# Kernel optimization log

Hardware: AMD Instinct MI355X
Metric: run time of the kernel (lower is better)

The kernel has to match this reference:

```python
import jax, jax.numpy as jnp
import numpy as np

N = 10000      # nodes
E = 160000     # edges
D_IN = 512
D_H = 512
P_DROP = 0.2


def _glorot(key, shape):
    lim = float(np.sqrt(6.0 / (shape[0] + shape[1])))
    return jax.random.uniform(key, shape, jnp.float32, -lim, lim)


def setup_inputs() -> dict:
    key = jax.random.key(0)
    ks = jax.random.split(key, 8)
    h = jax.random.normal(ks[0], (N, D_IN), jnp.float32)
    src = jax.random.randint(ks[1], (E,), 0, N)
    dst = jax.random.randint(ks[2], (E,), 0, N)
    edge_weight = jax.random.uniform(ks[3], (E,), jnp.float32)
    W0 = _glorot(ks[4], (D_IN, D_H))
    W1 = _glorot(ks[5], (D_H, D_H))
    W2 = _glorot(ks[6], (D_H, D_H))
    b0 = jnp.zeros((D_H,), jnp.float32)
    b1 = jnp.zeros((D_H,), jnp.float32)
    b2 = jnp.zeros((D_H,), jnp.float32)
    return dict(h=h, src=src, dst=dst, edge_weight=edge_weight,
                W0=W0, b0=b0, W1=W1, b1=b1, W2=W2, b2=b2)


def _dropout(x, key):
    keep = jax.random.bernoulli(key, 1.0 - P_DROP, x.shape)
    return jnp.where(keep, x / (1.0 - P_DROP), 0.0)


def _graph_conv(x, src, dst, ew, W, b, act):
    # DGL GraphConv, norm='both', weight=True, bias=True, with edge_weight.
    ones = jnp.ones((src.shape[0],), x.dtype)
    deg_out = jnp.maximum(jax.ops.segment_sum(ones, src, num_segments=N), 1.0)
    deg_in = jnp.maximum(jax.ops.segment_sum(ones, dst, num_segments=N), 1.0)
    x = x * (deg_out ** -0.5)[:, None]          # src norm
    msg = x[src] * ew[:, None]                  # [E, D] gather + edge weight
    agg = jax.ops.segment_sum(msg, dst, num_segments=N)  # scatter-add
    out = (agg @ W) * (deg_in ** -0.5)[:, None] + b
    return act(out) if act is not None else out


def reference(h, src, dst, edge_weight, W0, b0, W1, b1, W2, b2):
    dk = jax.random.split(jax.random.key(42), 3)
    x = _dropout(h, dk[0])
    x = _graph_conv(x, src, dst, edge_weight, W0, b0, jax.nn.elu)
    x = _dropout(x, dk[1])
    x = _graph_conv(x, src, dst, edge_weight, W1, b1, jax.nn.elu)
    x = _dropout(x, dk[2])
    x = _graph_conv(x, src, dst, edge_weight, W2, b2, None)
    return x
```

## Files before the change

### kernel.cpp

```cpp
#include <hip/hip_runtime.h>
#include <stdint.h>

#define N_NODES 10000
#define N_EDGES 160000
#define D 512
#define TOT (N_NODES * D)
#define NMASK (TOT / 32)
#define CAP 64
#define MT 32
#define NBLK_F 313
#define LDA3 520
#define LDB 40

typedef _Float16 h8 __attribute__((ext_vector_type(8)));
typedef float f4 __attribute__((ext_vector_type(4)));

__host__ __device__ inline uint32_t rotl32(uint32_t v, int r) {
    return (v << r) | (v >> (32 - r));
}

__host__ __device__ inline void tf2x32(uint32_t k0, uint32_t k1,
                                       uint32_t& x0, uint32_t& x1) {
    uint32_t k2 = k0 ^ k1 ^ 0x1BD11BDAu;
    x0 += k0; x1 += k1;
    x0 += x1; x1 = rotl32(x1, 13); x1 ^= x0;
    x0 += x1; x1 = rotl32(x1, 15); x1 ^= x0;
    x0 += x1; x1 = rotl32(x1, 26); x1 ^= x0;
    x0 += x1; x1 = rotl32(x1,  6); x1 ^= x0;
    x0 += k1; x1 += k2 + 1u;
    x0 += x1; x1 = rotl32(x1, 17); x1 ^= x0;
    x0 += x1; x1 = rotl32(x1, 29); x1 ^= x0;
    x0 += x1; x1 = rotl32(x1, 16); x1 ^= x0;
    x0 += x1; x1 = rotl32(x1, 24); x1 ^= x0;
    x0 += k2; x1 += k0 + 2u;
    x0 += x1; x1 = rotl32(x1, 13); x1 ^= x0;
    x0 += x1; x1 = rotl32(x1, 15); x1 ^= x0;
    x0 += x1; x1 = rotl32(x1, 26); x1 ^= x0;
    x0 += x1; x1 = rotl32(x1,  6); x1 ^= x0;
    x0 += k0; x1 += k1 + 3u;
    x0 += x1; x1 = rotl32(x1, 17); x1 ^= x0;
    x0 += x1; x1 = rotl32(x1, 29); x1 ^= x0;
    x0 += x1; x1 = rotl32(x1, 16); x1 ^= x0;
    x0 += x1; x1 = rotl32(x1, 24); x1 ^= x0;
    x0 += k1; x1 += k2 + 4u;
    x0 += x1; x1 = rotl32(x1, 13); x1 ^= x0;
    x0 += x1; x1 = rotl32(x1, 15); x1 ^= x0;
    x0 += x1; x1 = rotl32(x1, 26); x1 ^= x0;
    x0 += x1; x1 = rotl32(x1,  6); x1 ^= x0;
    x0 += k2; x1 += k0 + 5u;
}

__device__ __forceinline__ uint32_t dropout_bit(uint32_t k0, uint32_t k1, uint32_t j) {
    uint32_t c0 = 0u, c1 = j;
    tf2x32(k0, k1, c0, c1);
    uint32_t bits = c0 ^ c1;
    float u = __uint_as_float((bits >> 9) | 0x3f800000u) - 1.0f;
    return (u < 0.8f) ? 1u : 0u;
}

#define HIST_BLKS 625
#define WCONV_BLKS 192
#define DROP_BLKS 5000
#define MASKG_BLKS 625
#define PRE_BLKS (HIST_BLKS + WCONV_BLKS + DROP_BLKS + 2 * MASKG_BLKS)
__global__ __launch_bounds__(256)
void pre_kernel(const int* __restrict__ src, int* __restrict__ deg_out,
                const float* __restrict__ W0, const float* __restrict__ W1,
                const float* __restrict__ W2, _Float16* __restrict__ Wt,
                const float* __restrict__ x, _Float16* __restrict__ y,
                uint32_t k0, uint32_t k1,
                uint32_t m1k0, uint32_t m1k1, uint32_t* __restrict__ mask1,
                uint32_t m2k0, uint32_t m2k1, uint32_t* __restrict__ mask2) {
    __shared__ float tile[64][65];
    int b = blockIdx.x;
    int t = threadIdx.x;
    if (b < HIST_BLKS) {
        int e = b * 256 + t;
        atomicAdd(&deg_out[src[e]], 1);
    } else if (b < HIST_BLKS + WCONV_BLKS) {
        int b2 = b - HIST_BLKS;
        int bx = b2 & 7, by = (b2 >> 3) & 7, bz = b2 >> 6;
        const float* W = (bz == 0) ? W0 : (bz == 1) ? W1 : W2;
        _Float16* T = Wt + (size_t)bz * 512 * 512;
        int r0 = by * 64, c0 = bx * 64;
        int c = t & 63, rq = t >> 6;
#pragma unroll
        for (int i = 0; i < 16; ++i) {
            int r = rq + i * 4;
            tile[r][c] = W[(size_t)(r0 + r) * 512 + c0 + c];
        }
        __syncthreads();
        int k = t & 63, nq = t >> 6;
#pragma unroll
        for (int i = 0; i < 16; ++i) {
            int n = nq + i * 4;
            T[(size_t)(c0 + n) * 512 + r0 + k] = (_Float16)tile[k][n];
        }
    } else if (b < HIST_BLKS + WCONV_BLKS + DROP_BLKS) {
        int b3 = b - HIST_BLKS - WCONV_BLKS;
        int j = (b3 * 256 + t) * 4;
        if (j >= TOT) return;
        float4 xv = *(const float4*)&x[j];
        _Float16 r[4];
        uint32_t jj = (uint32_t)j;
#pragma unroll
        for (int i = 0; i < 4; ++i) {
            float g = dropout_bit(k0, k1, jj + (uint32_t)i) ? 1.0f : 0.0f;
            float xi = (&xv.x)[i];
            r[i] = (_Float16)(g * (xi * 1.25f));
        }
        *(ushort4*)&y[j] = *(ushort4*)r;
    } else {
        int b4 = b - HIST_BLKS - WCONV_BLKS - DROP_BLKS;
        int which = b4 / MASKG_BLKS;
        int gtid = (b4 % MASKG_BLKS) * 256 + t;
        uint32_t mk0 = which ? m2k0 : m1k0;
        uint32_t mk1 = which ? m2k1 : m1k1;
        uint32_t* m = which ? mask2 : mask1;
        uint32_t w = 0, jb = (uint32_t)gtid * 32u;
#pragma unroll 4
        for (int i = 0; i < 32; ++i)
            w |= dropout_bit(mk0, mk1, jb + (uint32_t)i) << i;
        m[gtid] = w;
    }
}

__global__ __launch_bounds__(256)
void fill_kernel(const int* __restrict__ src, const int* __restrict__ dst,
                 const float* __restrict__ ew, const int* __restrict__ deg_out,
                 int* __restrict__ cnt_in, int2* __restrict__ ell) {
    int e = blockIdx.x * 256 + threadIdx.x;
    int v = dst[e];
    int sn = src[e];
    int pos = atomicAdd(&cnt_in[v], 1);
    float rno = 1.0f / sqrtf(fmaxf((float)deg_out[sn], 1.0f));
    if (pos < CAP)
        ell[(size_t)v * CAP + pos] = make_int2(sn, __float_as_int(ew[e] * rno));
}

__global__ __launch_bounds__(512, 4)
void fused_layer(const _Float16* __restrict__ yin, const int* __restrict__ cnt_in,
                 const int2* __restrict__ ell, const _Float16* __restrict__ Wt,
                 const float* __restrict__ bias, const uint32_t* __restrict__ mask,
                 _Float16* __restrict__ yout, float* __restrict__ fout, int mode) {
    __shared__ _Float16 AT[MT * LDA3];
    __shared__ _Float16 Bs[512 * LDB];
    const int tid = threadIdx.x;
    const int w = tid >> 6, lane = tid & 63;
    const int base = blockIdx.x * MT;
    const _Float16* yl = yin + lane * 8;

    for (int i = 0; i < 4; ++i) {
        int row = w * 4 + i;
        int node = base + row;
        int deg = (node < N_NODES) ? cnt_in[node] : 0;
        if (deg > CAP) deg = CAP;
        const int2* ep = ell + (size_t)node * CAP;
        float acc[8] = {0, 0, 0, 0, 0, 0, 0, 0};
        int k = 0;
        for (; k + 15 < deg; k += 16) {
            int2 e[16];
#pragma unroll
            for (int u = 0; u < 16; ++u) e[u] = ep[k + u];
            h8 v[16];
#pragma unroll
            for (int u = 0; u < 16; ++u) v[u] = *(const h8*)&yl[(size_t)e[u].x * 512];
#pragma unroll
            for (int u = 0; u < 16; ++u) {
                float wt = __int_as_float(e[u].y);
#pragma unroll
                for (int j = 0; j < 8; ++j) acc[j] += wt * (float)v[u][j];
            }
        }
        for (; k + 3 < deg; k += 4) {
            int2 e[4];
#pragma unroll
            for (int u = 0; u < 4; ++u) e[u] = ep[k + u];
            h8 v[4];
#pragma unroll
            for (int u = 0; u < 4; ++u) v[u] = *(const h8*)&yl[(size_t)e[u].x * 512];
#pragma unroll
            for (int u = 0; u < 4; ++u) {
                float wt = __int_as_float(e[u].y);
#pragma unroll
                for (int j = 0; j < 8; ++j) acc[j] += wt * (float)v[u][j];
            }
        }
        for (; k < deg; ++k) {
            int2 e0 = ep[k];
            float wt = __int_as_float(e0.y);
            h8 v = *(const h8*)&yl[(size_t)e0.x * 512];
#pragma unroll
            for (int j = 0; j < 8; ++j) acc[j] += wt * (float)v[j];
        }
        _Float16 r[8];
#pragma unroll
        for (int j = 0; j < 8; ++j) r[j] = (_Float16)acc[j];
        *(h8*)&AT[row * LDA3 + lane * 8] = *(h8*)r;
    }
    __syncthreads();

    const int mq = w & 1, nq = w >> 1;
    f4 acc[8];
#pragma unroll
    for (int i = 0; i < 8; ++i) acc[i] = (f4){0.f, 0.f, 0.f, 0.f};

    const _Float16* wrow = Wt + (size_t)tid * 512;
    _Float16* bw = &Bs[tid * LDB];
    const _Float16* arow = &AT[(mq * 16 + (lane & 15)) * LDA3 + (lane >> 4) * 8];
    const _Float16* brow = &Bs[(nq * 128 + (lane & 15)) * LDB + (lane >> 4) * 8];

    h8 rb0 = *(const h8*)(wrow + 0);
    h8 rb1 = *(const h8*)(wrow + 8);
    h8 rb2 = *(const h8*)(wrow + 16);
    h8 rb3 = *(const h8*)(wrow + 24);

    for (int ks = 0; ks < 16; ++ks) {
        *(h8*)(bw + 0)  = rb0;
        *(h8*)(bw + 8)  = rb1;
        *(h8*)(bw + 16) = rb2;
        *(h8*)(bw + 24) = rb3;
        __syncthreads();
        if (ks < 15) {
            const _Float16* nx = wrow + (ks + 1) * 32;
            rb0 = *(const h8*)(nx + 0);
            rb1 = *(const h8*)(nx + 8);
            rb2 = *(const h8*)(nx + 16);
            rb3 = *(const h8*)(nx + 24);
        }
        h8 a = *(const h8*)(arow + ks * 32);
#pragma unroll
        for (int nt = 0; nt < 8; ++nt) {
            h8 bf = *(const h8*)(brow + nt * 16 * LDB);
            acc[nt] = __builtin_amdgcn_mfma_f32_16x16x32_f16(a, bf, acc[nt], 0, 0, 0);
        }
        __syncthreads();
    }

    const int r0g = (lane >> 4) * 4;
    float rn[4];
#pragma unroll
    for (int i = 0; i < 4; ++i) {
        int gr = base + mq * 16 + r0g + i;
        int d = (gr < N_NODES) ? cnt_in[gr] : 1;
        rn[i] = 1.0f / sqrtf(fmaxf((float)d, 1.0f));
    }
#pragma unroll
    for (int nt = 0; nt < 8; ++nt) {
        int col = nq * 128 + nt * 16 + (lane & 15);
        float bcol = bias[col];
#pragma unroll
        for (int i = 0; i < 4; ++i) {
            int gr = base + mq * 16 + r0g + i;
            if (gr >= N_NODES) continue;
            float v = acc[nt][i] * rn[i] + bcol;
            if (mode == 0) {
                v = (v > 0.f) ? v : (__expf(v) - 1.0f);
                uint32_t j = (uint32_t)(gr * 512 + col);
                uint32_t g = (mask[j >> 5] >> (j & 31)) & 1u;
                v = g ? (v * 1.25f) : 0.0f;
                AT[(mq * 16 + r0g + i) * LDA3 + col] = (_Float16)v;
            } else {
                fout[(size_t)gr * 512 + col] = v;
            }
        }
    }

    if (mode == 0) {
        __syncthreads();
#pragma unroll
        for (int i = 0; i < 4; ++i) {
            int c = tid + 512 * i;
            int row = c >> 6, col8 = c & 63;
            int gr = base + row;
            if (gr < N_NODES)
                *(h8*)&yout[(size_t)gr * 512 + col8 * 8] =
                    *(const h8*)&AT[row * LDA3 + col8 * 8];
        }
    }
}

extern "C" void kernel_launch(void* const* d_in, const int* in_sizes, int n_in,
                              void* d_out, int out_size, void* d_ws, size_t ws_size,
                              hipStream_t stream) {
    const float* x   = (const float*)d_in[0];
    const int*   src = (const int*)d_in[1];
    const int*   dst = (const int*)d_in[2];
    const float* ew  = (const float*)d_in[3];
    const float* W0  = (const float*)d_in[4];
    const float* b0  = (const float*)d_in[5];
    const float* W1  = (const float*)d_in[6];
    const float* b1  = (const float*)d_in[7];
    const float* W2  = (const float*)d_in[8];
    const float* b2  = (const float*)d_in[9];
    float* out = (float*)d_out;

    char* ws = (char*)d_ws;
    _Float16* y16  = (_Float16*)ws; ws += (size_t)TOT * 2;
    _Float16* y16b = (_Float16*)ws; ws += (size_t)TOT * 2;
    _Float16* Wt   = (_Float16*)ws; ws += (size_t)3 * 512 * 512 * 2;
    int* deg_out = (int*)ws;   ws += N_NODES * 4;
    int* cnt_in  = (int*)ws;   ws += N_NODES * 4;
    ws = (char*)(((uintptr_t)ws + 15) & ~(uintptr_t)15);
    int2* ell    = (int2*)ws;  ws += (size_t)N_NODES * CAP * 8;
    uint32_t* mask1 = (uint32_t*)ws; ws += (size_t)NMASK * 4;
    uint32_t* mask2 = (uint32_t*)ws; ws += (size_t)NMASK * 4;

    uint32_t dk[3][2];
    for (int i = 0; i < 3; ++i) {
        uint32_t c0 = 0u, c1 = (uint32_t)i;
        tf2x32(0u, 42u, c0, c1);
        dk[i][0] = c0; dk[i][1] = c1;
    }

    hipMemsetAsync(deg_out, 0, 2 * N_NODES * 4, stream);

    pre_kernel<<<PRE_BLKS, 256, 0, stream>>>(src, deg_out, W0, W1, W2, Wt,
                                             x, y16, dk[0][0], dk[0][1],
                                             dk[1][0], dk[1][1], mask1,
                                             dk[2][0], dk[2][1], mask2);
    fill_kernel<<<N_EDGES / 256, 256, 0, stream>>>(src, dst, ew, deg_out,
                                                   cnt_in, ell);

    fused_layer<<<NBLK_F, 512, 0, stream>>>(y16, cnt_in, ell, Wt,
                                            b0, mask1, y16b, nullptr, 0);
    fused_layer<<<NBLK_F, 512, 0, stream>>>(y16b, cnt_in, ell, Wt + (size_t)512 * 512,
                                            b1, mask2, y16, nullptr, 0);
    fused_layer<<<NBLK_F, 512, 0, stream>>>(y16, cnt_in, ell, Wt + (size_t)2 * 512 * 512,
                                            b2, nullptr, nullptr, out, 1);
}
```

Baseline: 325.3 us.

## Halve fused-layer row tile, merge degree histogram into ELL fill, swizzle B tile

Cuts the fused aggregation+GEMM tile from 32 to 16 rows with 256-thread blocks (625 blocks), so each wave owns a 128-column slice and loads two weight rows per stage into an XOR-swizzled unpadded LDS tile. The out-degree histogram moves into the ELL fill kernel, and the memset is replaced by zeroing blocks in the first pre-kernel. This removes one launch and the separate histogram pass. The cost is that the source norm is now recomputed per edge inside each layer from deg_out, adding a dependent gather per edge. Smaller tiles also mean every weight matrix is streamed twice as often.

```diff
diff --git a/kernel.cpp b/kernel.cpp
--- a/kernel.cpp
+++ b/kernel.cpp
@@ -7,10 +7,9 @@
 #define TOT (N_NODES * D)
 #define NMASK (TOT / 32)
 #define CAP 64
-#define MT 32
-#define NBLK_F 313
+#define MT 16
+#define NBLK_F 625
 #define LDA3 520
-#define LDB 40
 
 typedef _Float16 h8 __attribute__((ext_vector_type(8)));
 typedef float f4 __attribute__((ext_vector_type(4)));
@@ -58,27 +57,28 @@
     return (u < 0.8f) ? 1u : 0u;
 }
 
-#define HIST_BLKS 625
+#define ZERO_BLKS 20
 #define WCONV_BLKS 192
 #define DROP_BLKS 5000
 #define MASKG_BLKS 625
-#define PRE_BLKS (HIST_BLKS + WCONV_BLKS + DROP_BLKS + 2 * MASKG_BLKS)
+#define PRE1_BLKS (ZERO_BLKS + WCONV_BLKS + DROP_BLKS + 2 * MASKG_BLKS)
 __global__ __launch_bounds__(256)
-void pre_kernel(const int* __restrict__ src, int* __restrict__ deg_out,
-                const float* __restrict__ W0, const float* __restrict__ W1,
-                const float* __restrict__ W2, _Float16* __restrict__ Wt,
-                const float* __restrict__ x, _Float16* __restrict__ y,
-                uint32_t k0, uint32_t k1,
-                uint32_t m1k0, uint32_t m1k1, uint32_t* __restrict__ mask1,
-                uint32_t m2k0, uint32_t m2k1, uint32_t* __restrict__ mask2) {
+void pre1_kernel(int* __restrict__ zero_base,
+                 const float* __restrict__ W0, const float* __restrict__ W1,
+                 const float* __restrict__ W2, _Float16* __restrict__ Wt,
+                 const float* __restrict__ x, _Float16* __restrict__ y,
+                 uint32_t k0, uint32_t k1,
+                 uint32_t m1k0, uint32_t m1k1, uint32_t* __restrict__ mask1,
+                 uint32_t m2k0, uint32_t m2k1, uint32_t* __restrict__ mask2) {
     __shared__ float tile[64][65];
     int b = blockIdx.x;
     int t = threadIdx.x;
-    if (b < HIST_BLKS) {
-        int e = b * 256 + t;
-        atomicAdd(&deg_out[src[e]], 1);
-    } else if (b < HIST_BLKS + WCONV_BLKS) {
-        int b2 = b - HIST_BLKS;
+    if (b < ZERO_BLKS) {
+        int i = b * 256 + t;
+        if (i < 5000)
+            *(int4*)&zero_base[i * 4] = make_int4(0, 0, 0, 0);
+    } else if (b < ZERO_BLKS + WCONV_BLKS) {
+        int b2 = b - ZERO_BLKS;
         int bx = b2 & 7, by = (b2 >> 3) & 7, bz = b2 >> 6;
         const float* W = (bz == 0) ? W0 : (bz == 1) ? W1 : W2;
         _Float16* T = Wt + (size_t)bz * 512 * 512;
@@ -96,8 +96,8 @@
             int n = nq + i * 4;
             T[(size_t)(c0 + n) * 512 + r0 + k] = (_Float16)tile[k][n];
         }
-    } else if (b < HIST_BLKS + WCONV_BLKS + DROP_BLKS) {
-        int b3 = b - HIST_BLKS - WCONV_BLKS;
+    } else if (b < ZERO_BLKS + WCONV_BLKS + DROP_BLKS) {
+        int b3 = b - ZERO_BLKS - WCONV_BLKS;
         int j = (b3 * 256 + t) * 4;
         if (j >= TOT) return;
         float4 xv = *(const float4*)&x[j];
@@ -111,7 +111,7 @@
         }
         *(ushort4*)&y[j] = *(ushort4*)r;
     } else {
-        int b4 = b - HIST_BLKS - WCONV_BLKS - DROP_BLKS;
+        int b4 = b - ZERO_BLKS - WCONV_BLKS - DROP_BLKS;
         int which = b4 / MASKG_BLKS;
         int gtid = (b4 % MASKG_BLKS) * 256 + t;
         uint32_t mk0 = which ? m2k0 : m1k0;
@@ -126,25 +126,26 @@
 }
 
 __global__ __launch_bounds__(256)
-void fill_kernel(const int* __restrict__ src, const int* __restrict__ dst,
-                 const float* __restrict__ ew, const int* __restrict__ deg_out,
+void pre2_kernel(const int* __restrict__ src, const int* __restrict__ dst,
+                 const float* __restrict__ ew, int* __restrict__ deg_out,
                  int* __restrict__ cnt_in, int2* __restrict__ ell) {
     int e = blockIdx.x * 256 + threadIdx.x;
+    int sn = src[e];
     int v = dst[e];
-    int sn = src[e];
+    atomicAdd(&deg_out[sn], 1);
     int pos = atomicAdd(&cnt_in[v], 1);
-    float rno = 1.0f / sqrtf(fmaxf((float)deg_out[sn], 1.0f));
     if (pos < CAP)
-        ell[(size_t)v * CAP + pos] = make_int2(sn, __float_as_int(ew[e] * rno));
-}
-
-__global__ __launch_bounds__(512, 4)
-void fused_layer(const _Float16* __restrict__ yin, const int* __restrict__ cnt_in,
-                 const int2* __restrict__ ell, const _Float16* __restrict__ Wt,
-                 const float* __restrict__ bias, const uint32_t* __restrict__ mask,
+        ell[(size_t)v * CAP + pos] = make_int2(sn, __float_as_int(ew[e]));
+}
+
+__global__ __launch_bounds__(256, 3)
+void fused_layer(const _Float16* __restrict__ yin, const int* __restrict__ deg_out,
+                 const int* __restrict__ cnt_in, const int2* __restrict__ ell,
+                 const _Float16* __restrict__ Wt, const float* __restrict__ bias,
+                 const uint32_t* __restrict__ mask,
                  _Float16* __restrict__ yout, float* __restrict__ fout, int mode) {
     __shared__ _Float16 AT[MT * LDA3];
-    __shared__ _Float16 Bs[512 * LDB];
+    __shared__ _Float16 Bs[512 * 32];
     const int tid = threadIdx.x;
     const int w = tid >> 6, lane = tid & 63;
     const int base = blockIdx.x * MT;
@@ -153,7 +154,7 @@
     for (int i = 0; i < 4; ++i) {
         int row = w * 4 + i;
         int node = base + row;
-        int deg = (node < N_NODES) ? cnt_in[node] : 0;
+        int deg = cnt_in[node];
         if (deg > CAP) deg = CAP;
         const int2* ep = ell + (size_t)node * CAP;
         float acc[8] = {0, 0, 0, 0, 0, 0, 0, 0};
@@ -165,9 +166,13 @@
             h8 v[16];
 #pragma unroll
             for (int u = 0; u < 16; ++u) v[u] = *(const h8*)&yl[(size_t)e[u].x * 512];
+            float rno[16];
+#pragma unroll
+            for (int u = 0; u < 16; ++u)
+                rno[u] = 1.0f / sqrtf(fmaxf((float)deg_out[e[u].x], 1.0f));
 #pragma unroll
             for (int u = 0; u < 16; ++u) {
-                float wt = __int_as_float(e[u].y);
+                float wt = __int_as_float(e[u].y) * rno[u];
 #pragma unroll
                 for (int j = 0; j < 8; ++j) acc[j] += wt * (float)v[u][j];
             }
@@ -181,14 +186,16 @@
             for (int u = 0; u < 4; ++u) v[u] = *(const h8*)&yl[(size_t)e[u].x * 512];
 #pragma unroll
             for (int u = 0; u < 4; ++u) {
-                float wt = __int_as_float(e[u].y);
+                float wt = __int_as_float(e[u].y)
+                         * (1.0f / sqrtf(fmaxf((float)deg_out[e[u].x], 1.0f)));
 #pragma unroll
                 for (int j = 0; j < 8; ++j) acc[j] += wt * (float)v[u][j];
             }
         }
         for (; k < deg; ++k) {
             int2 e0 = ep[k];
-            float wt = __int_as_float(e0.y);
+            float wt = __int_as_float(e0.y)
+                     * (1.0f / sqrtf(fmaxf((float)deg_out[e0.x], 1.0f)));
             h8 v = *(const h8*)&yl[(size_t)e0.x * 512];
 #pragma unroll
             for (int j = 0; j < 8; ++j) acc[j] += wt * (float)v[j];
@@ -200,38 +207,46 @@
     }
     __syncthreads();
 
-    const int mq = w & 1, nq = w >> 1;
     f4 acc[8];
 #pragma unroll
     for (int i = 0; i < 8; ++i) acc[i] = (f4){0.f, 0.f, 0.f, 0.f};
 
-    const _Float16* wrow = Wt + (size_t)tid * 512;
-    _Float16* bw = &Bs[tid * LDB];
-    const _Float16* arow = &AT[(mq * 16 + (lane & 15)) * LDA3 + (lane >> 4) * 8];
-    const _Float16* brow = &Bs[(nq * 128 + (lane & 15)) * LDB + (lane >> 4) * 8];
-
-    h8 rb0 = *(const h8*)(wrow + 0);
-    h8 rb1 = *(const h8*)(wrow + 8);
-    h8 rb2 = *(const h8*)(wrow + 16);
-    h8 rb3 = *(const h8*)(wrow + 24);
-
+    const _Float16* w0 = Wt + (size_t)tid * 512;
+    const _Float16* w1 = Wt + (size_t)(tid + 256) * 512;
+    const int sw = (tid >> 1) & 3;
+    _Float16* bw0 = &Bs[tid * 32];
+    _Float16* bw1 = &Bs[(tid + 256) * 32];
+    const _Float16* arow = &AT[(lane & 15) * LDA3 + (lane >> 4) * 8];
+
+    h8 rb0[4], rb1[4];
+#pragma unroll
+    for (int c = 0; c < 4; ++c) {
+        rb0[c] = *(const h8*)(w0 + c * 8);
+        rb1[c] = *(const h8*)(w1 + c * 8);
+    }
+
+    const int kc = lane >> 4;
     for (int ks = 0; ks < 16; ++ks) {
-        *(h8*)(bw + 0)  = rb0;
-        *(h8*)(bw + 8)  = rb1;
-        *(h8*)(bw + 16) = rb2;
-        *(h8*)(bw + 24) = rb3;
+#pragma unroll
+        for (int c = 0; c < 4; ++c) {
+            *(h8*)(bw0 + (c ^ sw) * 8) = rb0[c];
+            *(h8*)(bw1 + (c ^ sw) * 8) = rb1[c];
+        }
         __syncthreads();
         if (ks < 15) {
-            const _Float16* nx = wrow + (ks + 1) * 32;
-            rb0 = *(const h8*)(nx + 0);
-            rb1 = *(const h8*)(nx + 8);
-            rb2 = *(const h8*)(nx + 16);
-            rb3 = *(const h8*)(nx + 24);
+            const _Float16* n0 = w0 + (ks + 1) * 32;
+            const _Float16* n1 = w1 + (ks + 1) * 32;
+#pragma unroll
+            for (int c = 0; c < 4; ++c) {
+                rb0[c] = *(const h8*)(n0 + c * 8);
+                rb1[c] = *(const h8*)(n1 + c * 8);
+            }
         }
         h8 a = *(const h8*)(arow + ks * 32);
 #pragma unroll
         for (int nt = 0; nt < 8; ++nt) {
-            h8 bf = *(const h8*)(brow + nt * 16 * LDB);
+            int col = w * 128 + nt * 16 + (lane & 15);
+            h8 bf = *(const h8*)&Bs[col * 32 + ((kc ^ ((col >> 1) & 3)) * 8)];
             acc[nt] = __builtin_amdgcn_mfma_f32_16x16x32_f16(a, bf, acc[nt], 0, 0, 0);
         }
         __syncthreads();
@@ -241,25 +256,23 @@
     float rn[4];
 #pragma unroll
     for (int i = 0; i < 4; ++i) {
-        int gr = base + mq * 16 + r0g + i;
-        int d = (gr < N_NODES) ? cnt_in[gr] : 1;
+        int d = cnt_in[base + r0g + i];
         rn[i] = 1.0f / sqrtf(fmaxf((float)d, 1.0f));
     }
 #pragma unroll
     for (int nt = 0; nt < 8; ++nt) {
-        int col = nq * 128 + nt * 16 + (lane & 15);
+        int col = w * 128 + nt * 16 + (lane & 15);
         float bcol = bias[col];
 #pragma unroll
         for (int i = 0; i < 4; ++i) {
-            int gr = base + mq * 16 + r0g + i;
-            if (gr >= N_NODES) continue;
+            int gr = base + r0g + i;
             float v = acc[nt][i] * rn[i] + bcol;
             if (mode == 0) {
                 v = (v > 0.f) ? v : (__expf(v) - 1.0f);
                 uint32_t j = (uint32_t)(gr * 512 + col);
                 uint32_t g = (mask[j >> 5] >> (j & 31)) & 1u;
                 v = g ? (v * 1.25f) : 0.0f;
-                AT[(mq * 16 + r0g + i) * LDA3 + col] = (_Float16)v;
+                AT[(r0g + i) * LDA3 + col] = (_Float16)v;
             } else {
                 fout[(size_t)gr * 512 + col] = v;
             }
@@ -270,12 +283,10 @@
         __syncthreads();
 #pragma unroll
         for (int i = 0; i < 4; ++i) {
-            int c = tid + 512 * i;
+            int c = tid + 256 * i;
             int row = c >> 6, col8 = c & 63;
-            int gr = base + row;
-            if (gr < N_NODES)
-                *(h8*)&yout[(size_t)gr * 512 + col8 * 8] =
-                    *(const h8*)&AT[row * LDA3 + col8 * 8];
+            *(h8*)&yout[(size_t)(base + row) * 512 + col8 * 8] =
+                *(const h8*)&AT[row * LDA3 + col8 * 8];
         }
     }
 }
@@ -313,19 +324,19 @@
         dk[i][0] = c0; dk[i][1] = c1;
     }
 
-    hipMemsetAsync(deg_out, 0, 2 * N_NODES * 4, stream);
-
-    pre_kernel<<<PRE_BLKS, 256, 0, stream>>>(src, deg_out, W0, W1, W2, Wt,
-                                             x, y16, dk[0][0], dk[0][1],
-                                             dk[1][0], dk[1][1], mask1,
-                                             dk[2][0], dk[2][1], mask2);
-    fill_kernel<<<N_EDGES / 256, 256, 0, stream>>>(src, dst, ew, deg_out,
+    pre1_kernel<<<PRE1_BLKS, 256, 0, stream>>>(deg_out, W0, W1, W2, Wt,
+                                               x, y16, dk[0][0], dk[0][1],
+                                               dk[1][0], dk[1][1], mask1,
+                                               dk[2][0], dk[2][1], mask2);
+    pre2_kernel<<<N_EDGES / 256, 256, 0, stream>>>(src, dst, ew, deg_out,
                                                    cnt_in, ell);
 
-    fused_layer<<<NBLK_F, 512, 0, stream>>>(y16, cnt_in, ell, Wt,
+    fused_layer<<<NBLK_F, 256, 0, stream>>>(y16, deg_out, cnt_in, ell, Wt,
                                             b0, mask1, y16b, nullptr, 0);
-    fused_layer<<<NBLK_F, 512, 0, stream>>>(y16b, cnt_in, ell, Wt + (size_t)512 * 512,
+    fused_layer<<<NBLK_F, 256, 0, stream>>>(y16b, deg_out, cnt_in, ell,
+                                            Wt + (size_t)512 * 512,
                                             b1, mask2, y16, nullptr, 0);
-    fused_layer<<<NBLK_F, 512, 0, stream>>>(y16, cnt_in, ell, Wt + (size_t)2 * 512 * 512,
+    fused_layer<<<NBLK_F, 256, 0, stream>>>(y16, deg_out, cnt_in, ell,
+                                            Wt + (size_t)2 * 512 * 512,
                                             b2, nullptr, nullptr, out, 1);
 }
```

New measurement: 399.0 us. 1.23x slower.
